# Kernel optimization log

Measured on AMD Instinct MI355X. Metric: run time of the kernel, lower is better.

## Reference

```python
import jax, jax.numpy as jnp
import numpy as np

NEG_SLOPE = 0.2  # LeakyReLU slope from the source module


def setup_inputs() -> dict:
    key = jax.random.key(0)
    k_x, k_adj, k_w, k_a = jax.random.split(key, 4)
    N, F_in, F_out, H = 4096, 256, 512, 8
    d = F_out // H
    x = jax.random.normal(k_x, (N, F_in), dtype=jnp.float32)
    adj = jax.random.randint(k_adj, (N, N), 0, 2, dtype=jnp.int32)  # unused by forward, faithful to source
    W = jax.random.normal(k_w, (F_out, F_in), dtype=jnp.float32) * 0.05  # nn.Linear weight [out, in], bias=False
    A = jax.random.normal(k_a, (H, d, d), dtype=jnp.float32) * 0.05      # per-head bilinear attention
    return {"x": x, "adj": adj, "W": W, "A": A}


def reference(x, adj, W, A):
    # x: [N, F_in], W: [F_out, F_in], A: [H, d, d] with F_out = H*d. adj is unused (as in source forward).
    N = x.shape[0]
    H, d, _ = A.shape
    h = (x @ W.T).reshape(N, H, d)                        # [N, H, d]
    q = jnp.einsum('nhd,hde->nhe', h, A)                  # attn_for_self: bilinear projection
    e = jnp.einsum('nhe,mhe->nhm', q, h)                  # attn_for_neighs: [N, H, N] raw scores
    e = jnp.where(e >= 0, e, NEG_SLOPE * e)               # LeakyReLU(0.2)
    attn = jax.nn.softmax(e, axis=-1)                     # normalize over neighbor nodes
    out = jnp.einsum('nhm,mhd->nhd', attn, h)             # weighted neighbor aggregation
    return out.reshape(N, H * d)
```

## Files before the change

### kernel.cpp

```cpp
#include <hip/hip_runtime.h>
#include <stdint.h>


typedef short bf16x8 __attribute__((ext_vector_type(8)));
typedef short short4v __attribute__((ext_vector_type(4)));
typedef float f32x4 __attribute__((ext_vector_type(4)));

#define LOG2E 1.4426950408889634f

__device__ __forceinline__ short f2bf(float f) {
  union { float f; unsigned u; } x;
  x.f = f;
  unsigned r = (x.u + 0x7FFFu + ((x.u >> 16) & 1u)) >> 16;
  return (short)r;
}
__device__ __forceinline__ unsigned pack2(float f0, float f1) {
  union { float f; unsigned u; } a, b;
  a.f = f0; b.f = f1;
  return ((a.u + 0x8000u) >> 16) | ((b.u + 0x8000u) & 0xFFFF0000u);
}

__global__ __launch_bounds__(256) void prep(const float* __restrict__ xf,
                                            const float* __restrict__ W,
                                            const float* __restrict__ A,
                                            short* __restrict__ xb,
                                            short* __restrict__ Wc) {
  const int b = blockIdx.x;
  if (b < 1024) {
    const int i = (b * 256 + threadIdx.x) * 4;
    float4 v = *(const float4*)(xf + i);
    short4v s = {f2bf(v.x), f2bf(v.y), f2bf(v.z), f2bf(v.w)};
    *(short4v*)(xb + i) = s;
  } else {
    const int r = b - 1024;
    const int k = threadIdx.x;
    if (r < 512) {
      Wc[r * 256 + k] = f2bf(W[r * 256 + k]);
    } else {
      const int rr = r - 512;
      const int head = rr >> 6, e = rr & 63;
      float acc = 0.f;
      for (int dd = 0; dd < 64; ++dd) {
        acc += A[(head * 64 + dd) * 64 + e] * W[(head * 64 + dd) * 256 + k];
      }
      Wc[r * 256 + k] = f2bf(acc * LOG2E);
    }
  }
}

__global__ __launch_bounds__(256) void gemm_hqT(const short* __restrict__ x,
                                                const short* __restrict__ Wc,
                                                short* __restrict__ hq,
                                                short* __restrict__ hT) {
  __shared__ short T[64 * 65];
  const int tid = threadIdx.x;
  const int wave = tid >> 6, lane = tid & 63;
  const int quad = lane >> 4, c = lane & 15;
  const int row0 = blockIdx.y * 64 + wave * 16;
  const int col0 = blockIdx.x * 64;

  f32x4 acc[4];
#pragma unroll
  for (int nt = 0; nt < 4; ++nt) acc[nt] = (f32x4){0.f, 0.f, 0.f, 0.f};
#pragma unroll
  for (int ks = 0; ks < 8; ++ks) {
    bf16x8 a = *(const bf16x8*)(x + (row0 + c) * 256 + ks * 32 + quad * 8);
#pragma unroll
    for (int nt = 0; nt < 4; ++nt) {
      bf16x8 b = *(const bf16x8*)(Wc + (col0 + nt * 16 + c) * 256 + ks * 32 + quad * 8);
      acc[nt] = __builtin_amdgcn_mfma_f32_16x16x32_bf16(a, b, acc[nt], 0, 0, 0);
    }
  }
#pragma unroll
  for (int nt = 0; nt < 4; ++nt)
#pragma unroll
    for (int r = 0; r < 4; ++r) {
      const short v = f2bf(acc[nt][r]);
      hq[(row0 + quad * 4 + r) * 1024 + col0 + nt * 16 + c] = v;
      T[(wave * 16 + quad * 4 + r) * 65 + nt * 16 + c] = v;
    }

  if (blockIdx.x < 8) {
    __syncthreads();
    const int fl = tid >> 2, nch = (tid & 3) * 16;
    short vals[16];
#pragma unroll
    for (int i = 0; i < 16; ++i) vals[i] = T[(nch + i) * 65 + fl];
    bf16x8 lo = {vals[0], vals[1], vals[2], vals[3], vals[4], vals[5], vals[6], vals[7]};
    bf16x8 hi = {vals[8], vals[9], vals[10], vals[11], vals[12], vals[13], vals[14], vals[15]};
    short* dst = hT + (col0 + fl) * 4096 + blockIdx.y * 64 + nch;
    *(bf16x8*)dst = lo;
    *(bf16x8*)(dst + 8) = hi;
  }
}

__global__ __launch_bounds__(256, 4) void attn_split(const short* __restrict__ hq,
                                                     const short* __restrict__ hT,
                                                     short* __restrict__ po,
                                                     float* __restrict__ pl) {
  const int tid = threadIdx.x;
  const int wave = tid >> 6, lane = tid & 63;
  const int quad = lane >> 4, c = lane & 15;
  const int head = blockIdx.y;
  const int q0 = blockIdx.x * 128 + wave * 32;

  __shared__ __align__(16) short K_lds[64 * 68];
  __shared__ __align__(16) short Vt_lds[64 * 68];
  __shared__ __align__(16) short P_lds[4 * 32 * 68];
  short* Pw = &P_lds[wave * 32 * 68];

  bf16x8 qf[2][2];
#pragma unroll
  for (int p = 0; p < 2; ++p) {
    const short* qb = hq + (q0 + p * 16 + c) * 1024 + 512 + head * 64 + quad * 8;
    qf[p][0] = *(const bf16x8*)qb;
    qf[p][1] = *(const bf16x8*)(qb + 32);
  }
  const short one = (short)0x3F80;
  const bf16x8 ones = {one, one, one, one, one, one, one, one};

  f32x4 o[2][4], ol[2];
#pragma unroll
  for (int p = 0; p < 2; ++p) {
#pragma unroll
    for (int mt = 0; mt < 4; ++mt) o[p][mt] = (f32x4){0.f, 0.f, 0.f, 0.f};
    ol[p] = (f32x4){0.f, 0.f, 0.f, 0.f};
  }

  const int kt0 = blockIdx.z * 16;
  for (int kt = kt0; kt < kt0 + 16; ++kt) {
    __syncthreads();
#pragma unroll
    for (int pp = 0; pp < 2; ++pp) {
      const int chunk = tid + pp * 256;
      const int key = chunk >> 3, dc = chunk & 7;
      bf16x8 v = *(const bf16x8*)(hq + (kt * 64 + key) * 1024 + head * 64 + dc * 8);
      *(bf16x8*)&K_lds[key * 68 + dc * 8] = v;
      bf16x8 w = *(const bf16x8*)(hT + (head * 64 + key) * 4096 + kt * 64 + dc * 8);
      *(bf16x8*)&Vt_lds[key * 68 + dc * 8] = w;
    }
    __syncthreads();

#pragma unroll
    for (int mt = 0; mt < 4; ++mt) {
      bf16x8 a0 = *(const bf16x8*)&K_lds[(mt * 16 + c) * 68 + quad * 8];
      bf16x8 a1 = *(const bf16x8*)&K_lds[(mt * 16 + c) * 68 + 32 + quad * 8];
#pragma unroll
      for (int p = 0; p < 2; ++p) {
        f32x4 s = (f32x4){0.f, 0.f, 0.f, 0.f};
        s = __builtin_amdgcn_mfma_f32_16x16x32_bf16(a0, qf[p][0], s, 0, 0, 0);
        s = __builtin_amdgcn_mfma_f32_16x16x32_bf16(a1, qf[p][1], s, 0, 0, 0);
        const float p0 = exp2f(fmaxf(s[0], 0.2f * s[0]));
        const float p1 = exp2f(fmaxf(s[1], 0.2f * s[1]));
        const float p2 = exp2f(fmaxf(s[2], 0.2f * s[2]));
        const float p3 = exp2f(fmaxf(s[3], 0.2f * s[3]));
        uint2 d = {pack2(p0, p1), pack2(p2, p3)};
        *(uint2*)&Pw[(p * 16 + c) * 68 + mt * 16 + quad * 4] = d;
      }
    }
    bf16x8 pb[2][2];
#pragma unroll
    for (int p = 0; p < 2; ++p) {
      short4v r0 = *(const short4v*)&Pw[(p * 16 + c) * 68 + quad * 8];
      short4v r1 = *(const short4v*)&Pw[(p * 16 + c) * 68 + quad * 8 + 4];
      short4v r2 = *(const short4v*)&Pw[(p * 16 + c) * 68 + 32 + quad * 8];
      short4v r3 = *(const short4v*)&Pw[(p * 16 + c) * 68 + 32 + quad * 8 + 4];
      pb[p][0] = (bf16x8){r0[0], r0[1], r0[2], r0[3], r1[0], r1[1], r1[2], r1[3]};
      pb[p][1] = (bf16x8){r2[0], r2[1], r2[2], r2[3], r3[0], r3[1], r3[2], r3[3]};
    }
#pragma unroll
    for (int mt = 0; mt < 4; ++mt) {
      bf16x8 va0 = *(const bf16x8*)&Vt_lds[(mt * 16 + c) * 68 + quad * 8];
      bf16x8 va1 = *(const bf16x8*)&Vt_lds[(mt * 16 + c) * 68 + 32 + quad * 8];
#pragma unroll
      for (int p = 0; p < 2; ++p) {
        o[p][mt] = __builtin_amdgcn_mfma_f32_16x16x32_bf16(va0, pb[p][0], o[p][mt], 0, 0, 0);
        o[p][mt] = __builtin_amdgcn_mfma_f32_16x16x32_bf16(va1, pb[p][1], o[p][mt], 0, 0, 0);
      }
    }
#pragma unroll
    for (int p = 0; p < 2; ++p) {
      ol[p] = __builtin_amdgcn_mfma_f32_16x16x32_bf16(ones, pb[p][0], ol[p], 0, 0, 0);
      ol[p] = __builtin_amdgcn_mfma_f32_16x16x32_bf16(ones, pb[p][1], ol[p], 0, 0, 0);
    }
  }

  const int pbi = (blockIdx.x * 8 + blockIdx.y) * 4 + blockIdx.z;
  short* po_b = po + (size_t)pbi * 8192;
#pragma unroll
  for (int p = 0; p < 2; ++p) {
    const int ql = wave * 32 + p * 16 + c;
#pragma unroll
    for (int mt = 0; mt < 4; ++mt) {
      short4v o4 = {f2bf(o[p][mt][0]), f2bf(o[p][mt][1]),
                    f2bf(o[p][mt][2]), f2bf(o[p][mt][3])};
      *(short4v*)&po_b[ql * 64 + mt * 16 + quad * 4] = o4;
    }
    if (quad == 0) pl[pbi * 128 + ql] = ol[p][0];
  }
}

__global__ __launch_bounds__(256) void merge4(const short* __restrict__ po,
                                              const float* __restrict__ pl,
                                              float* __restrict__ out) {
  const int qt = blockIdx.x, head = blockIdx.y, t = threadIdx.x;
  const int q = t >> 2, dg = t & 3;
  const int q128 = (qt & 1) * 64 + q;
  const int pbb = ((qt >> 1) * 8 + head) * 4;
  const float inv = 1.0f / (pl[pbb * 128 + q128] + pl[(pbb + 1) * 128 + q128] +
                            pl[(pbb + 2) * 128 + q128] + pl[(pbb + 3) * 128 + q128]);
  float a[16];
#pragma unroll
  for (int i = 0; i < 16; ++i) a[i] = 0.f;
#pragma unroll
  for (int z = 0; z < 4; ++z) {
    const short* p = po + (size_t)(pbb + z) * 8192 + q128 * 64 + dg * 16;
    bf16x8 lo = *(const bf16x8*)p;
    bf16x8 hi = *(const bf16x8*)(p + 8);
#pragma unroll
    for (int i = 0; i < 8; ++i) {
      union { unsigned u; float f; } x, y;
      x.u = ((unsigned)(unsigned short)lo[i]) << 16;
      y.u = ((unsigned)(unsigned short)hi[i]) << 16;
      a[i] += x.f;
      a[i + 8] += y.f;
    }
  }
  float* op = out + (qt * 64 + q) * 512 + head * 64 + dg * 16;
#pragma unroll
  for (int i = 0; i < 4; ++i) {
    float4 r = {a[i * 4] * inv, a[i * 4 + 1] * inv, a[i * 4 + 2] * inv, a[i * 4 + 3] * inv};
    *(float4*)(op + i * 4) = r;
  }
}

extern "C" void kernel_launch(void* const* d_in, const int* in_sizes, int n_in,
                              void* d_out, int out_size, void* d_ws, size_t ws_size,
                              hipStream_t stream) {
  const float* x = (const float*)d_in[0];
  const float* W = (const float*)d_in[2];
  const float* A = (const float*)d_in[3];
  for (int i = 0; i < n_in; ++i) {
    if (in_sizes[i] == 4096 * 256) x = (const float*)d_in[i];
    else if (in_sizes[i] == 512 * 256) W = (const float*)d_in[i];
    else if (in_sizes[i] == 8 * 64 * 64) A = (const float*)d_in[i];
  }

  float* out = (float*)d_out;
  short* xb = (short*)d_ws;
  short* Wc = xb + 4096 * 256;
  short* hq = Wc + 1024 * 256;
  short* hT = hq + 4096 * 1024;
  short* po = hT + 512 * 4096;
  float* pl = (float*)(po + (size_t)1024 * 8192);

  prep<<<dim3(2048), dim3(256), 0, stream>>>(x, W, A, xb, Wc);
  gemm_hqT<<<dim3(16, 64), dim3(256), 0, stream>>>(xb, Wc, hq, hT);
  attn_split<<<dim3(32, 8, 4), dim3(256), 0, stream>>>(hq, hT, po, pl);
  merge4<<<dim3(64, 8), dim3(256), 0, stream>>>(po, pl, out);
}
```

Before: 200.1 us.

## Prefetch next K/V tile into registers and use native exp2 and bf16 pack

Global loads for the next key/value tile now go into registers while the current tile is being computed, so global memory latency overlaps with the MFMA and softmax work. The library exp2f is replaced with the raw v_exp_f32 instruction, and the manual bf16 rounding pack is replaced with the v_cvt_pk_bf16_f32 instruction. In exchange, register pressure rises, the final iteration does one redundant reload, and exp2 loses the library's denormal and range handling.

```diff
diff --git a/kernel.cpp b/kernel.cpp
--- a/kernel.cpp
+++ b/kernel.cpp
@@ -14,10 +14,21 @@
   unsigned r = (x.u + 0x7FFFu + ((x.u >> 16) & 1u)) >> 16;
   return (short)r;
 }
-__device__ __forceinline__ unsigned pack2(float f0, float f1) {
-  union { float f; unsigned u; } a, b;
-  a.f = f0; b.f = f1;
-  return ((a.u + 0x8000u) >> 16) | ((b.u + 0x8000u) & 0xFFFF0000u);
+
+__device__ __forceinline__ float rexp2(float x) {
+#if __has_builtin(__builtin_amdgcn_exp2f)
+  return __builtin_amdgcn_exp2f(x);
+#else
+  float r;
+  asm("v_exp_f32 %0, %1" : "=v"(r) : "v"(x));
+  return r;
+#endif
+}
+
+__device__ __forceinline__ unsigned cvtpk(float lo, float hi) {
+  unsigned r;
+  asm("v_cvt_pk_bf16_f32 %0, %1, %2" : "=v"(r) : "v"(lo), "v"(hi));
+  return r;
 }
 
 __global__ __launch_bounds__(256) void prep(const float* __restrict__ xf,
@@ -128,17 +139,32 @@
   }
 
   const int kt0 = blockIdx.z * 16;
+
+  const int chunk0 = tid, chunk1 = tid + 256;
+  const int key0 = chunk0 >> 3, dc0 = chunk0 & 7;
+  const int key1 = chunk1 >> 3, dc1 = chunk1 & 7;
+  const short* kp0 = hq + (size_t)(kt0 * 64 + key0) * 1024 + head * 64 + dc0 * 8;
+  const short* kp1 = hq + (size_t)(kt0 * 64 + key1) * 1024 + head * 64 + dc1 * 8;
+  const short* vp0 = hT + (size_t)(head * 64 + key0) * 4096 + kt0 * 64 + dc0 * 8;
+  const short* vp1 = hT + (size_t)(head * 64 + key1) * 4096 + kt0 * 64 + dc1 * 8;
+  bf16x8 kr0 = *(const bf16x8*)kp0;
+  bf16x8 kr1 = *(const bf16x8*)kp1;
+  bf16x8 vr0 = *(const bf16x8*)vp0;
+  bf16x8 vr1 = *(const bf16x8*)vp1;
+
   for (int kt = kt0; kt < kt0 + 16; ++kt) {
     __syncthreads();
-#pragma unroll
-    for (int pp = 0; pp < 2; ++pp) {
-      const int chunk = tid + pp * 256;
-      const int key = chunk >> 3, dc = chunk & 7;
-      bf16x8 v = *(const bf16x8*)(hq + (kt * 64 + key) * 1024 + head * 64 + dc * 8);
-      *(bf16x8*)&K_lds[key * 68 + dc * 8] = v;
-      bf16x8 w = *(const bf16x8*)(hT + (head * 64 + key) * 4096 + kt * 64 + dc * 8);
-      *(bf16x8*)&Vt_lds[key * 68 + dc * 8] = w;
-    }
+    *(bf16x8*)&K_lds[key0 * 68 + dc0 * 8] = kr0;
+    *(bf16x8*)&K_lds[key1 * 68 + dc1 * 8] = kr1;
+    *(bf16x8*)&Vt_lds[key0 * 68 + dc0 * 8] = vr0;
+    *(bf16x8*)&Vt_lds[key1 * 68 + dc1 * 8] = vr1;
+    const int adv = (kt + 1 < kt0 + 16) ? 1 : 0;
+    kp0 += adv * 65536; kp1 += adv * 65536;
+    vp0 += adv * 64;    vp1 += adv * 64;
+    kr0 = *(const bf16x8*)kp0;
+    kr1 = *(const bf16x8*)kp1;
+    vr0 = *(const bf16x8*)vp0;
+    vr1 = *(const bf16x8*)vp1;
     __syncthreads();
 
 #pragma unroll
@@ -150,11 +176,11 @@
         f32x4 s = (f32x4){0.f, 0.f, 0.f, 0.f};
         s = __builtin_amdgcn_mfma_f32_16x16x32_bf16(a0, qf[p][0], s, 0, 0, 0);
         s = __builtin_amdgcn_mfma_f32_16x16x32_bf16(a1, qf[p][1], s, 0, 0, 0);
-        const float p0 = exp2f(fmaxf(s[0], 0.2f * s[0]));
-        const float p1 = exp2f(fmaxf(s[1], 0.2f * s[1]));
-        const float p2 = exp2f(fmaxf(s[2], 0.2f * s[2]));
-        const float p3 = exp2f(fmaxf(s[3], 0.2f * s[3]));
-        uint2 d = {pack2(p0, p1), pack2(p2, p3)};
+        const float p0 = rexp2(fmaxf(s[0], 0.2f * s[0]));
+        const float p1 = rexp2(fmaxf(s[1], 0.2f * s[1]));
+        const float p2 = rexp2(fmaxf(s[2], 0.2f * s[2]));
+        const float p3 = rexp2(fmaxf(s[3], 0.2f * s[3]));
+        uint2 d = {cvtpk(p0, p1), cvtpk(p2, p3)};
         *(uint2*)&Pw[(p * 16 + c) * 68 + mt * 16 + quad * 4] = d;
       }
     }
```

After: 178.2 us. -10.9%, faster.
